# Optimization experiments

Hardware: AMD Instinct MI355X
Metric: run time of the kernel (lower is better)

The kernel has to match this reference:

```python
import jax, jax.numpy as jnp
import numpy as np

N_NODES = 100000
N_EDGES = 1600000
F_IN = 32
HIDDEN = 32
N_CLASSES = 2


def setup_inputs() -> dict:
    key = jax.random.key(0)
    k0, k1, k2, k3 = jax.random.split(key, 4)
    x = jax.random.normal(k0, (N_NODES, F_IN), dtype=jnp.float32)
    edge_index = jax.random.randint(k1, (2, N_EDGES), 0, N_NODES, dtype=jnp.int64)
    W1 = jax.random.normal(k2, (F_IN, HIDDEN), dtype=jnp.float32) / np.sqrt(F_IN).astype(np.float32)
    b1 = jnp.zeros((HIDDEN,), dtype=jnp.float32)
    W2 = jax.random.normal(k3, (HIDDEN, N_CLASSES), dtype=jnp.float32) / np.sqrt(HIDDEN).astype(np.float32)
    b2 = jnp.zeros((N_CLASSES,), dtype=jnp.float32)
    return {"x": x, "edge_index": edge_index, "W1": W1, "b1": b1, "W2": W2, "b2": b2}


def _gcn_conv(x, W, b, src, dst, norm, n):
    # linear transform, gather from source nodes, scale by sym-norm, scatter-add to dst
    msg = (x @ W)[src] * norm[:, None]  # [E+N, out]
    return jax.ops.segment_sum(msg, dst, num_segments=n) + b


def reference(x, edge_index, W1, b1, W2, b2):
    n = x.shape[0]
    loops = jnp.arange(n, dtype=edge_index.dtype)
    src = jnp.concatenate([edge_index[0], loops])  # add self-loops (GCNConv default)
    dst = jnp.concatenate([edge_index[1], loops])
    deg = jax.ops.segment_sum(jnp.ones_like(dst, dtype=jnp.float32), dst, num_segments=n)
    dis = jax.lax.rsqrt(jnp.maximum(deg, 1.0))  # deg >= 1 because of self-loops
    norm = dis[src] * dis[dst]  # D^{-1/2} A_hat D^{-1/2} edge weights
    h = jax.nn.relu(_gcn_conv(x, W1, b1, src, dst, norm, n))
    # dropout is identity in eval mode (training=False)
    out = _gcn_conv(h, W2, b2, src, dst, norm, n)
    return jax.nn.log_softmax(out, axis=1)
```

## Files before the change

kernel.cpp:

```cpp
#include <hip/hip_runtime.h>
#include <hip/hip_fp16.h>
#include <math.h>

constexpr int N = 100000;
constexpr int E = 1600000;
constexpr int F = 32;
constexpr int C = 2;

constexpr int NBUCK = (N + 511) >> 9;
constexpr int CAPB  = 10240;
constexpr int CHUNK = 8192;
constexpr int NCHUNK = (E + CHUNK - 1) / CHUNK;

__global__ void k_detect(const int* __restrict__ ei, int* __restrict__ flag,
                         int* __restrict__ bcursor) {
    __shared__ int any;
    if (threadIdx.x == 0) any = 0;
    __syncthreads();
    int acc = 0;
    for (int i = threadIdx.x; i < 2048; i += blockDim.x)
        acc |= ei[2 * i + 1];
    if (acc) atomicOr(&any, 1);
    for (int i = threadIdx.x; i < NBUCK; i += blockDim.x) bcursor[i] = 0;
    __syncthreads();
    if (threadIdx.x == 0) flag[0] = any ? 0 : 1;
}

__device__ __forceinline__ int get_src(const int* ei, int e, int f64) {
    return f64 ? ei[2 * e] : ei[e];
}
__device__ __forceinline__ int get_dst(const int* ei, int e, int f64) {
    return f64 ? ei[2 * (E + e)] : ei[E + e];
}

__global__ void k_bucket(const int* __restrict__ ei, int* __restrict__ bcursor,
                         int* __restrict__ epk, const int* __restrict__ flag) {
    __shared__ int h[NBUCK];
    __shared__ int base[NBUCK];
    __shared__ int sS[CHUNK];
    __shared__ int sD[CHUNK];
    int tid = threadIdx.x;
    for (int i = tid; i < NBUCK; i += blockDim.x) h[i] = 0;
    __syncthreads();
    int f64 = flag[0];
    int e0 = blockIdx.x * CHUNK;
    int ne = min(E - e0, CHUNK);
    for (int i = tid; i < ne; i += blockDim.x) {
        int s = get_src(ei, e0 + i, f64);
        int d = get_dst(ei, e0 + i, f64);
        sS[i] = s;
        sD[i] = d;
        atomicAdd(&h[d >> 9], 1);
    }
    __syncthreads();
    for (int b = tid; b < NBUCK; b += blockDim.x) {
        if (h[b] > 0) base[b] = atomicAdd(&bcursor[b], h[b]);
        h[b] = 0;
    }
    __syncthreads();
    for (int i = tid; i < ne; i += blockDim.x) {
        int d = sD[i];
        int b = d >> 9;
        int r = atomicAdd(&h[b], 1);
        int pos = base[b] + r;
        if (pos < CAPB)
            epk[b * CAPB + pos] = ((d & 511) << 17) | sS[i];
    }
}

__global__ __launch_bounds__(512) void k_csr(
        const int* __restrict__ epk, const int* __restrict__ bcursor,
        int* __restrict__ rs, int* __restrict__ re,
        float* __restrict__ dis, int* __restrict__ colp) {
    __shared__ int hcnt[512];
    __shared__ int s[512];
    __shared__ int lcur[512];
    __shared__ int colseg[CAPB];
    int b = blockIdx.x;
    int tid = threadIdx.x;
    int n0 = b << 9;
    int nn = min(512, N - n0);
    int cbase = b * CAPB;
    int cnt = min(bcursor[b], CAPB);
    hcnt[tid] = 0;
    __syncthreads();
    for (int i = tid; i < cnt; i += 512)
        atomicAdd(&hcnt[epk[cbase + i] >> 17], 1);
    __syncthreads();
    s[tid] = hcnt[tid];
    __syncthreads();
    for (int off = 1; off < 512; off <<= 1) {
        int t = (tid >= off) ? s[tid - off] : 0;
        __syncthreads();
        s[tid] += t;
        __syncthreads();
    }
    int excl = s[tid] - hcnt[tid];
    lcur[tid] = excl;
    if (tid < nn) {
        rs[n0 + tid] = cbase + excl;
        re[n0 + tid] = cbase + excl + hcnt[tid];
        dis[n0 + tid] = rsqrtf((float)(hcnt[tid] + 1));
    }
    __syncthreads();
    for (int i = tid; i < cnt; i += 512) {
        int p = epk[cbase + i];
        int r = atomicAdd(&lcur[p >> 17], 1);
        colseg[r] = p & 0x1FFFF;
    }
    __syncthreads();
    for (int i = tid; i < cnt; i += 512) colp[cbase + i] = colseg[i];
}

__global__ void k_xw1(const float* __restrict__ x, const float* __restrict__ W1,
                      const float* __restrict__ dis, __half* __restrict__ t1h) {
    __shared__ float W1s[F * F];
    int tid = threadIdx.x;
    for (int i = tid; i < F * F; i += blockDim.x) W1s[i] = W1[i];
    __syncthreads();
    int lane = tid & 31;
    int node = (blockIdx.x * blockDim.x + tid) >> 5;
    if (node >= N) return;
    float xv = x[node * F + lane];
    float acc = 0.f;
#pragma unroll
    for (int k = 0; k < F; ++k) acc += __shfl(xv, k, 32) * W1s[k * F + lane];
    float v = acc * dis[node];
    float o = __shfl_xor(v, 1, 32);
    if (!(lane & 1))
        ((__half2*)t1h)[node * 16 + (lane >> 1)] = __floats2half2_rn(v, o);
}

__device__ __forceinline__ void acc8(float4& lo, float4& hi, const float4& r) {
    const __half2* hp = (const __half2*)&r;
    float2 f0 = __half22float2(hp[0]);
    float2 f1 = __half22float2(hp[1]);
    float2 f2 = __half22float2(hp[2]);
    float2 f3 = __half22float2(hp[3]);
    lo.x += f0.x; lo.y += f0.y; lo.z += f1.x; lo.w += f1.y;
    hi.x += f2.x; hi.y += f2.y; hi.z += f3.x; hi.w += f3.y;
}

__global__ void k_agg1(const int* __restrict__ rs, const int* __restrict__ re,
                       const int* __restrict__ colp, const __half* __restrict__ t1h,
                       const float* __restrict__ dis, const float* __restrict__ b1,
                       const float* __restrict__ W2, float* __restrict__ t2) {
    int tid = blockIdx.x * blockDim.x + threadIdx.x;
    int node = tid >> 2;
    if (node >= N) return;
    int lane = tid & 3;
    const float4* t1v = (const float4*)t1h;
    int start = rs[node], end = re[node];
    float4 lo0 = {0,0,0,0}, hi0 = {0,0,0,0};
    float4 lo1 = {0,0,0,0}, hi1 = {0,0,0,0};
    float4 lo2 = {0,0,0,0}, hi2 = {0,0,0,0};
    float4 lo3 = {0,0,0,0}, hi3 = {0,0,0,0};
    for (int base = start; base < end; base += 4) {
        int idx = base + lane;
        int sv = (idx < end) ? colp[idx] : 0;
        int cnt = end - base;
        if (cnt >= 4) {
            int i0 = __shfl(sv, 0, 4);
            int i1 = __shfl(sv, 1, 4);
            int i2 = __shfl(sv, 2, 4);
            int i3 = __shfl(sv, 3, 4);
            float4 r0 = t1v[i0 * 4 + lane];
            float4 r1 = t1v[i1 * 4 + lane];
            float4 r2 = t1v[i2 * 4 + lane];
            float4 r3 = t1v[i3 * 4 + lane];
            acc8(lo0, hi0, r0);
            acc8(lo1, hi1, r1);
            acc8(lo2, hi2, r2);
            acc8(lo3, hi3, r3);
        } else {
            for (int j = 0; j < cnt; ++j) {
                int ss = __shfl(sv, j, 4);
                float4 r = t1v[ss * 4 + lane];
                acc8(lo0, hi0, r);
            }
        }
    }
    float4 alo, ahi;
    alo.x = (lo0.x + lo1.x) + (lo2.x + lo3.x);
    alo.y = (lo0.y + lo1.y) + (lo2.y + lo3.y);
    alo.z = (lo0.z + lo1.z) + (lo2.z + lo3.z);
    alo.w = (lo0.w + lo1.w) + (lo2.w + lo3.w);
    ahi.x = (hi0.x + hi1.x) + (hi2.x + hi3.x);
    ahi.y = (hi0.y + hi1.y) + (hi2.y + hi3.y);
    ahi.z = (hi0.z + hi1.z) + (hi2.z + hi3.z);
    ahi.w = (hi0.w + hi1.w) + (hi2.w + hi3.w);
    float4 wself = t1v[node * 4 + lane];
    const __half2* sp = (const __half2*)&wself;
    float2 s0 = __half22float2(sp[0]);
    float2 s1 = __half22float2(sp[1]);
    float2 s2 = __half22float2(sp[2]);
    float2 s3 = __half22float2(sp[3]);
    float d = dis[node];
    int f0 = 8 * lane;
    float4 b1lo = *(const float4*)(b1 + f0);
    float4 b1hi = *(const float4*)(b1 + f0 + 4);
    float h0 = fmaxf(d * (alo.x + s0.x) + b1lo.x, 0.f);
    float h1 = fmaxf(d * (alo.y + s0.y) + b1lo.y, 0.f);
    float h2 = fmaxf(d * (alo.z + s1.x) + b1lo.z, 0.f);
    float h3 = fmaxf(d * (alo.w + s1.y) + b1lo.w, 0.f);
    float h4 = fmaxf(d * (ahi.x + s2.x) + b1hi.x, 0.f);
    float h5 = fmaxf(d * (ahi.y + s2.y) + b1hi.y, 0.f);
    float h6 = fmaxf(d * (ahi.z + s3.x) + b1hi.z, 0.f);
    float h7 = fmaxf(d * (ahi.w + s3.y) + b1hi.w, 0.f);
    const float4* w2v = (const float4*)W2;
    float4 q0 = w2v[4 * lane + 0];
    float4 q1 = w2v[4 * lane + 1];
    float4 q2 = w2v[4 * lane + 2];
    float4 q3 = w2v[4 * lane + 3];
    float p0 = h0 * q0.x + h1 * q0.z + h2 * q1.x + h3 * q1.z +
               h4 * q2.x + h5 * q2.z + h6 * q3.x + h7 * q3.z;
    float p1 = h0 * q0.y + h1 * q0.w + h2 * q1.y + h3 * q1.w +
               h4 * q2.y + h5 * q2.w + h6 * q3.y + h7 * q3.w;
    p0 += __shfl_xor(p0, 1, 4);
    p0 += __shfl_xor(p0, 2, 4);
    p1 += __shfl_xor(p1, 1, 4);
    p1 += __shfl_xor(p1, 2, 4);
    if (lane == 0) {
        float2 o;
        o.x = p0 * d;
        o.y = p1 * d;
        *(float2*)(t2 + node * C) = o;
    }
}

__global__ void k_agg2(const int* __restrict__ rs, const int* __restrict__ re,
                       const int* __restrict__ colp, const float* __restrict__ t2,
                       const float* __restrict__ dis, const float* __restrict__ b2,
                       float* __restrict__ out) {
    int tid = blockIdx.x * blockDim.x + threadIdx.x;
    int node = tid >> 4;
    if (node >= N) return;
    int lane = tid & 15;
    int start = rs[node], end = re[node];
    float a0 = 0.f, a1 = 0.f;
    for (int idx = start + lane; idx < end; idx += 16) {
        int s = colp[idx];
        float2 v = *(const float2*)(t2 + s * C);
        a0 += v.x;
        a1 += v.y;
    }
#pragma unroll
    for (int off = 8; off > 0; off >>= 1) {
        a0 += __shfl_xor(a0, off, 16);
        a1 += __shfl_xor(a1, off, 16);
    }
    if (lane == 0) {
        float d = dis[node];
        float2 self = *(const float2*)(t2 + node * C);
        float z0 = d * (a0 + self.x) + b2[0];
        float z1 = d * (a1 + self.y) + b2[1];
        float m = fmaxf(z0, z1);
        float l = m + logf(expf(z0 - m) + expf(z1 - m));
        float2 o;
        o.x = z0 - l;
        o.y = z1 - l;
        *(float2*)(out + node * C) = o;
    }
}

extern "C" void kernel_launch(void* const* d_in, const int* in_sizes, int n_in,
                              void* d_out, int out_size, void* d_ws, size_t ws_size,
                              hipStream_t stream) {
    const float* x  = (const float*)d_in[0];
    const int*   ei = (const int*)d_in[1];
    const float* W1 = (const float*)d_in[2];
    const float* b1 = (const float*)d_in[3];
    const float* W2 = (const float*)d_in[4];
    const float* b2 = (const float*)d_in[5];
    float* out = (float*)d_out;

    int* ws_i = (int*)d_ws;
    int*    epk     = ws_i;
    int*    colp    = epk + (size_t)NBUCK * CAPB;
    int*    rs      = colp + (size_t)NBUCK * CAPB;
    int*    re      = rs + N;
    float*  dis     = (float*)(re + N);
    float*  t2      = (float*)(dis + N);
    int*    bcursor = (int*)(t2 + (size_t)N * C);
    int*    flag    = bcursor + NBUCK;
    __half* t1h     = (__half*)epk;

    const int B = 256;
    k_detect<<<1, B, 0, stream>>>(ei, flag, bcursor);
    k_bucket<<<NCHUNK, B, 0, stream>>>(ei, bcursor, epk, flag);
    k_csr<<<NBUCK, 512, 0, stream>>>(epk, bcursor, rs, re, dis, colp);
    k_xw1<<<(N * 32 + B - 1) / B, B, 0, stream>>>(x, W1, dis, t1h);
    k_agg1<<<(N * 4 + B - 1) / B, B, 0, stream>>>(rs, re, colp, t1h, dis, b1, W2, t2);
    k_agg2<<<(N * 16 + B - 1) / B, B, 0, stream>>>(rs, re, colp, t2, dis, b2, out);
}
```

Baseline: 109.9 us.

## Fuse XW1 into CSR build, fold detect into bucket, split gather by source range

Removes the separate detect kernel: each bucket block now does its own int64-layout check, and a memset clears the cursors. The x@W1 transform moves into the CSR kernel, reusing the per-node degree histogram already in shared memory, which drops one launch and a round trip through the dis array. t1h now gets its own workspace region instead of aliasing epk. The layer-1 aggregation makes two passes over each node's edge list, each gathering only sources from one half of the node range, to improve cache locality of the gathered rows. The cost is reading the edge list twice and issuing masked dummy loads.

```diff
diff --git a/kernel.cpp b/kernel.cpp
--- a/kernel.cpp
+++ b/kernel.cpp
@@ -11,20 +11,7 @@
 constexpr int CAPB  = 10240;
 constexpr int CHUNK = 8192;
 constexpr int NCHUNK = (E + CHUNK - 1) / CHUNK;
-
-__global__ void k_detect(const int* __restrict__ ei, int* __restrict__ flag,
-                         int* __restrict__ bcursor) {
-    __shared__ int any;
-    if (threadIdx.x == 0) any = 0;
-    __syncthreads();
-    int acc = 0;
-    for (int i = threadIdx.x; i < 2048; i += blockDim.x)
-        acc |= ei[2 * i + 1];
-    if (acc) atomicOr(&any, 1);
-    for (int i = threadIdx.x; i < NBUCK; i += blockDim.x) bcursor[i] = 0;
-    __syncthreads();
-    if (threadIdx.x == 0) flag[0] = any ? 0 : 1;
-}
+constexpr int SPLIT = 50000;
 
 __device__ __forceinline__ int get_src(const int* ei, int e, int f64) {
     return f64 ? ei[2 * e] : ei[e];
@@ -34,15 +21,21 @@
 }
 
 __global__ void k_bucket(const int* __restrict__ ei, int* __restrict__ bcursor,
-                         int* __restrict__ epk, const int* __restrict__ flag) {
+                         int* __restrict__ epk) {
     __shared__ int h[NBUCK];
     __shared__ int base[NBUCK];
     __shared__ int sS[CHUNK];
     __shared__ int sD[CHUNK];
+    __shared__ int sflag;
     int tid = threadIdx.x;
+    if (tid == 0) sflag = 0;
     for (int i = tid; i < NBUCK; i += blockDim.x) h[i] = 0;
     __syncthreads();
-    int f64 = flag[0];
+    int accf = 0;
+    for (int i = tid; i < 2048; i += blockDim.x) accf |= ei[2 * i + 1];
+    if (accf) atomicOr(&sflag, 1);
+    __syncthreads();
+    int f64 = sflag ? 0 : 1;
     int e0 = blockIdx.x * CHUNK;
     int ne = min(E - e0, CHUNK);
     for (int i = tid; i < ne; i += blockDim.x) {
@@ -70,11 +63,14 @@
 
 __global__ __launch_bounds__(512) void k_csr(
         const int* __restrict__ epk, const int* __restrict__ bcursor,
+        const float* __restrict__ x, const float* __restrict__ W1,
         int* __restrict__ rs, int* __restrict__ re,
-        float* __restrict__ dis, int* __restrict__ colp) {
+        float* __restrict__ dis, int* __restrict__ colp,
+        __half* __restrict__ t1h) {
     __shared__ int hcnt[512];
     __shared__ int s[512];
     __shared__ int lcur[512];
+    __shared__ float W1s[F * F];
     __shared__ int colseg[CAPB];
     int b = blockIdx.x;
     int tid = threadIdx.x;
@@ -83,6 +79,7 @@
     int cbase = b * CAPB;
     int cnt = min(bcursor[b], CAPB);
     hcnt[tid] = 0;
+    for (int i = tid; i < F * F; i += 512) W1s[i] = W1[i];
     __syncthreads();
     for (int i = tid; i < cnt; i += 512)
         atomicAdd(&hcnt[epk[cbase + i] >> 17], 1);
@@ -110,25 +107,24 @@
     }
     __syncthreads();
     for (int i = tid; i < cnt; i += 512) colp[cbase + i] = colseg[i];
-}
-
-__global__ void k_xw1(const float* __restrict__ x, const float* __restrict__ W1,
-                      const float* __restrict__ dis, __half* __restrict__ t1h) {
-    __shared__ float W1s[F * F];
-    int tid = threadIdx.x;
-    for (int i = tid; i < F * F; i += blockDim.x) W1s[i] = W1[i];
-    __syncthreads();
+    int g = tid >> 5;
     int lane = tid & 31;
-    int node = (blockIdx.x * blockDim.x + tid) >> 5;
-    if (node >= N) return;
-    float xv = x[node * F + lane];
-    float acc = 0.f;
+    for (int it = 0; it < 32; ++it) {
+        int ln = (g << 5) + it;
+        if (ln < nn) {
+            float xv = x[(size_t)(n0 + ln) * F + lane];
+            float acc = 0.f;
 #pragma unroll
-    for (int k = 0; k < F; ++k) acc += __shfl(xv, k, 32) * W1s[k * F + lane];
-    float v = acc * dis[node];
-    float o = __shfl_xor(v, 1, 32);
-    if (!(lane & 1))
-        ((__half2*)t1h)[node * 16 + (lane >> 1)] = __floats2half2_rn(v, o);
+            for (int k = 0; k < F; ++k)
+                acc += __shfl(xv, k, 32) * W1s[k * F + lane];
+            float d = rsqrtf((float)(hcnt[ln] + 1));
+            float v = acc * d;
+            float o = __shfl_xor(v, 1, 32);
+            if (!(lane & 1))
+                ((__half2*)t1h)[(size_t)(n0 + ln) * 16 + (lane >> 1)] =
+                    __floats2half2_rn(v, o);
+        }
+    }
 }
 
 __device__ __forceinline__ void acc8(float4& lo, float4& hi, const float4& r) {
@@ -155,29 +151,33 @@
     float4 lo1 = {0,0,0,0}, hi1 = {0,0,0,0};
     float4 lo2 = {0,0,0,0}, hi2 = {0,0,0,0};
     float4 lo3 = {0,0,0,0}, hi3 = {0,0,0,0};
-    for (int base = start; base < end; base += 4) {
-        int idx = base + lane;
-        int sv = (idx < end) ? colp[idx] : 0;
-        int cnt = end - base;
-        if (cnt >= 4) {
+#pragma unroll 1
+    for (int pass = 0; pass < 2; ++pass) {
+        unsigned LO = pass ? SPLIT : 0u;
+        unsigned RG = pass ? (unsigned)(N - SPLIT) : (unsigned)SPLIT;
+        for (int base = start; base < end; base += 4) {
+            int idx = base + lane;
+            int sv = (idx < end) ? colp[idx] : -1;
             int i0 = __shfl(sv, 0, 4);
             int i1 = __shfl(sv, 1, 4);
             int i2 = __shfl(sv, 2, 4);
             int i3 = __shfl(sv, 3, 4);
-            float4 r0 = t1v[i0 * 4 + lane];
-            float4 r1 = t1v[i1 * 4 + lane];
-            float4 r2 = t1v[i2 * 4 + lane];
-            float4 r3 = t1v[i3 * 4 + lane];
-            acc8(lo0, hi0, r0);
-            acc8(lo1, hi1, r1);
-            acc8(lo2, hi2, r2);
-            acc8(lo3, hi3, r3);
-        } else {
-            for (int j = 0; j < cnt; ++j) {
-                int ss = __shfl(sv, j, 4);
-                float4 r = t1v[ss * 4 + lane];
-                acc8(lo0, hi0, r);
-            }
+            bool c0 = (unsigned)(i0 - LO) < RG;
+            bool c1 = (unsigned)(i1 - LO) < RG;
+            bool c2 = (unsigned)(i2 - LO) < RG;
+            bool c3 = (unsigned)(i3 - LO) < RG;
+            int j0 = c0 ? i0 : node;
+            int j1 = c1 ? i1 : node;
+            int j2 = c2 ? i2 : node;
+            int j3 = c3 ? i3 : node;
+            float4 r0 = t1v[j0 * 4 + lane];
+            float4 r1 = t1v[j1 * 4 + lane];
+            float4 r2 = t1v[j2 * 4 + lane];
+            float4 r3 = t1v[j3 * 4 + lane];
+            if (c0) acc8(lo0, hi0, r0);
+            if (c1) acc8(lo1, hi1, r1);
+            if (c2) acc8(lo2, hi2, r2);
+            if (c3) acc8(lo3, hi3, r3);
         }
     }
     float4 alo, ahi;
@@ -280,16 +280,14 @@
     int*    rs      = colp + (size_t)NBUCK * CAPB;
     int*    re      = rs + N;
     float*  dis     = (float*)(re + N);
-    float*  t2      = (float*)(dis + N);
+    __half* t1h     = (__half*)(dis + N);
+    float*  t2      = (float*)(t1h + (size_t)N * F);
     int*    bcursor = (int*)(t2 + (size_t)N * C);
-    int*    flag    = bcursor + NBUCK;
-    __half* t1h     = (__half*)epk;
 
     const int B = 256;
-    k_detect<<<1, B, 0, stream>>>(ei, flag, bcursor);
-    k_bucket<<<NCHUNK, B, 0, stream>>>(ei, bcursor, epk, flag);
-    k_csr<<<NBUCK, 512, 0, stream>>>(epk, bcursor, rs, re, dis, colp);
-    k_xw1<<<(N * 32 + B - 1) / B, B, 0, stream>>>(x, W1, dis, t1h);
+    hipMemsetAsync(bcursor, 0, NBUCK * sizeof(int), stream);
+    k_bucket<<<NCHUNK, B, 0, stream>>>(ei, bcursor, epk);
+    k_csr<<<NBUCK, 512, 0, stream>>>(epk, bcursor, x, W1, rs, re, dis, colp, t1h);
     k_agg1<<<(N * 4 + B - 1) / B, B, 0, stream>>>(rs, re, colp, t1h, dis, b1, W2, t2);
     k_agg2<<<(N * 16 + B - 1) / B, B, 0, stream>>>(rs, re, colp, t2, dis, b2, out);
 }
```

Measured after the change: 114.1 us. 3.9% more time.
